# Optimization experiments

Measured on AMD Instinct MI355X. Metric: run time of the kernel, lower is better.

Reference implementation:

```python
import jax, jax.numpy as jnp
import numpy as np

BLANK = 0
B, T, D_TN = 32, 1000, 640
D_PN, D_J, V = 640, 640, 1024


def lstm_step(x, h, c, W_ih, W_hh, b):
    # x:[B,D_PN] h,c:[B,D_PN]
    gates = x @ W_ih.T + h @ W_hh.T + b  # [B,4*D_PN]
    i, f, g, o = jnp.split(gates, 4, axis=-1)
    c_new = jax.nn.sigmoid(f) * c + jax.nn.sigmoid(i) * jnp.tanh(g)
    h_new = jax.nn.sigmoid(o) * jnp.tanh(c_new)
    return h_new, c_new


def setup_inputs() -> dict:
    key = jax.random.key(0)
    ks = jax.random.split(key, 10)
    s_pn = 1.0 / np.sqrt(D_PN)
    s_tn = 1.0 / np.sqrt(D_TN)
    s_j = 1.0 / np.sqrt(D_J)
    return {
        "tn_output": jax.random.normal(ks[0], (B, T, D_TN), jnp.float32),
        "E": jax.random.normal(ks[1], (V, D_PN), jnp.float32) * 0.02,
        "W_ih": jax.random.normal(ks[2], (4 * D_PN, D_PN), jnp.float32) * s_pn,
        "W_hh": jax.random.normal(ks[3], (4 * D_PN, D_PN), jnp.float32) * s_pn,
        "b_lstm": jnp.zeros((4 * D_PN,), jnp.float32),
        "W_tn": jax.random.normal(ks[4], (D_J, D_TN), jnp.float32) * s_tn,
        "W_pn": jax.random.normal(ks[5], (D_J, D_PN), jnp.float32) * s_pn,
        "b_joint": jnp.zeros((D_J,), jnp.float32),
        "W_out": jax.random.normal(ks[6], (V, D_J), jnp.float32) * s_j,
        "b_out": jnp.zeros((V,), jnp.float32),
    }


def reference(tn_output, E, W_ih, W_hh, b_lstm, W_tn, W_pn, b_joint, W_out, b_out):
    """Vectorized transducer greedy decode (beam_size=1 path).
    Returns (emitted_tokens [B,T] (blank where no emission), logp_scores [B],
    mean exp score scalar) mirroring the torch module's greedy output."""
    b, t = tn_output.shape[0], tn_output.shape[1]
    dt = tn_output.dtype
    # initial PN step on initial_token_id (= blank), hidden None -> zeros
    h0 = jnp.zeros((b, W_hh.shape[1]), dt)
    c0 = jnp.zeros((b, W_hh.shape[1]), dt)
    x0 = E[jnp.full((b,), BLANK)]
    h, c = lstm_step(x0, h0, c0, W_ih, W_hh, b_lstm)
    out_pn = h
    # precompute TN projection for the whole utterance: [T,B,D_J]
    tn_proj = jnp.einsum("btd,jd->tbj", tn_output, W_tn)

    def step(state, tn_t):
        h, c, out_pn, last_tok, score = state
        z = jnp.tanh(tn_t + out_pn @ W_pn.T + b_joint)          # [B,D_J]
        logp = jax.nn.log_softmax(z @ W_out.T + b_out, axis=-1)  # [B,V]
        pos = jnp.argmax(logp, axis=-1).astype(jnp.int32)        # [B]
        lp = jnp.take_along_axis(logp, pos[:, None].astype(jnp.int32), axis=-1)[:, 0]
        nonblank = pos != BLANK
        score = score + jnp.where(nonblank, lp, jnp.zeros_like(lp))
        tok = jnp.where(nonblank, pos, last_tok)
        # PN advances only for hyps that emitted a non-blank label
        h2, c2 = lstm_step(E[tok], h, c, W_ih, W_hh, b_lstm)
        m = nonblank[:, None]
        h_n = jnp.where(m, h2, h)
        c_n = jnp.where(m, c2, c)
        out_n = jnp.where(m, h2, out_pn)
        emit = jnp.where(nonblank, pos, jnp.full_like(pos, BLANK))
        return (h_n, c_n, out_n, tok, score), emit

    init = (h, c, out_pn, jnp.full((b,), BLANK, jnp.int32), jnp.zeros((b,), dt))
    (_, _, _, _, score), emits = jax.lax.scan(step, init, tn_proj)
    tokens = jnp.swapaxes(emits, 0, 1)  # [B,T]
    return tokens, score, jnp.exp(score).mean()
```

## Files before the change

### kernel.cpp

```cpp
#include <hip/hip_runtime.h>
#include <stdint.h>


typedef unsigned long long u64;
typedef uint32_t u32;

#define TT 1000
#define DD 640
#define GG 2560
#define VV 1024

#define NA 80
#define NL 64
#define NC 80
#define NBLK (NA + NL + NC)

static constexpr size_t OFF_WTN  = 0;
static constexpr size_t OFF_WPN  = OFF_WTN  + 409600;
static constexpr size_t OFF_WHH  = OFF_WPN  + 409600;
static constexpr size_t OFF_WOUT = OFF_WHH  + 1638400;
static constexpr size_t OFF_P    = OFF_WOUT + 655360;
static constexpr size_t OFF_XH   = OFF_P    + 2621440;
static constexpr size_t OFF_XZ   = OFF_XH   + 40960;
static constexpr size_t OFF_SC   = OFF_XZ   + 20480;
static constexpr size_t OFF_LKEY = OFF_SC   + 32;
static constexpr size_t OFF_LSE  = OFF_LKEY + 4096;
static constexpr size_t OFF_MCFC = OFF_LSE  + 2048;
static constexpr size_t OFF_MCFA = OFF_MCFC + 51200;
static constexpr size_t OFF_MCFL = OFF_MCFA + 20480;
static constexpr size_t OFF_END  = OFF_MCFL + 20480;

__device__ __forceinline__ float sigf(float x) { return 1.0f / (1.0f + expf(-x)); }

__device__ __forceinline__ u32 ordf(float f) {
  u32 u = __float_as_uint(f);
  return (u & 0x80000000u) ? ~u : (u | 0x80000000u);
}

__device__ __forceinline__ void cstore2(float* p, float a, float b) {
  u64 v = ((u64)__float_as_uint(b) << 32) | (u64)__float_as_uint(a);
  __hip_atomic_store((u64*)p, v, __ATOMIC_RELAXED, __HIP_MEMORY_SCOPE_AGENT);
}
__device__ __forceinline__ float2 cload2(const float* p) {
  u64 v = __hip_atomic_load((const u64*)p, __ATOMIC_RELAXED, __HIP_MEMORY_SCOPE_AGENT);
  return make_float2(__uint_as_float((u32)v), __uint_as_float((u32)(v >> 32)));
}
__device__ __forceinline__ u64 cloadu64(const u64* p) {
  return __hip_atomic_load(p, __ATOMIC_RELAXED, __HIP_MEMORY_SCOPE_AGENT);
}
__device__ __forceinline__ void cstoreu64(u64* p, u64 v) {
  __hip_atomic_store(p, v, __ATOMIC_RELAXED, __HIP_MEMORY_SCOPE_AGENT);
}
__device__ __forceinline__ float cloadf(const float* p) {
  return __hip_atomic_load(p, __ATOMIC_RELAXED, __HIP_MEMORY_SCOPE_AGENT);
}
__device__ __forceinline__ void cstoref(float* p, float v) {
  __hip_atomic_store(p, v, __ATOMIC_RELAXED, __HIP_MEMORY_SCOPE_AGENT);
}

__device__ __forceinline__ void wait_mc(const int* mc, int nprod, int target) {
  if ((int)threadIdx.x < nprod) {
    while (__hip_atomic_load(mc + threadIdx.x * 4, __ATOMIC_RELAXED,
                             __HIP_MEMORY_SCOPE_AGENT) < target)
      __builtin_amdgcn_s_sleep(2);
  }
  __syncthreads();
}
__device__ __forceinline__ void publish_mc(int* mc, int ncons, int nprod,
                                           int myprod, int val) {
  __syncthreads();
  if ((int)threadIdx.x < ncons)
    __hip_atomic_store(mc + ((size_t)threadIdx.x * nprod + myprod) * 4, val,
                       __ATOMIC_RELAXED, __HIP_MEMORY_SCOPE_AGENT);
}

__device__ __forceinline__ void fma4(float& a, const float4 w, const float4 x) {
  a = fmaf(w.x, x.x, fmaf(w.y, x.y, fmaf(w.z, x.z, fmaf(w.w, x.w, a))));
}
__device__ __forceinline__ void fma22(float& a, const float4 w, const float2 xa,
                                      const float2 xb) {
  a = fmaf(w.x, xa.x, fmaf(w.y, xa.y, fmaf(w.z, xb.x, fmaf(w.w, xb.y, a))));
}


__global__ __launch_bounds__(256) void k_wt4(const float* __restrict__ W,
                                             float* __restrict__ WT4, int J) {
  __shared__ float tile[64][65];
  int nj = J >> 6;
  int tj = blockIdx.x % nj, tk = blockIdx.x / nj;
  int jb = tj << 6, kb = tk << 6;
  for (int i = threadIdx.x; i < 4096; i += 256) {
    int d = i & 63, j = i >> 6;
    tile[j][d] = W[(size_t)(jb + j) * DD + (kb + d)];
  }
  __syncthreads();
  for (int i = threadIdx.x; i < 1024; i += 256) {
    int j = i & 63, q = i >> 6;
    float4 v = make_float4(tile[j][q * 4], tile[j][q * 4 + 1], tile[j][q * 4 + 2],
                           tile[j][q * 4 + 3]);
    ((float4*)WT4)[(size_t)((kb >> 2) + q) * J + (jb + j)] = v;
  }
}

__global__ __launch_bounds__(256) void k_pgemm(const float* __restrict__ E,
                                               const float* __restrict__ Wih,
                                               float* __restrict__ P) {
  __shared__ float As[16][65], Bs[16][65];
  int vt = blockIdx.x & 15, gt = blockIdx.x >> 4;
  int vb = vt << 6, gb = gt << 6;
  int tv = threadIdx.x & 15, tg = threadIdx.x >> 4;
  float acc[4][4] = {};
  for (int kb = 0; kb < DD; kb += 16) {
    for (int i = threadIdx.x; i < 1024; i += 256) {
      int k = i & 15, x = i >> 4;
      As[k][x] = E[(size_t)(vb + x) * DD + kb + k];
      Bs[k][x] = Wih[(size_t)(gb + x) * DD + kb + k];
    }
    __syncthreads();
#pragma unroll
    for (int k = 0; k < 16; ++k) {
      float av[4], bv[4];
#pragma unroll
      for (int i = 0; i < 4; ++i) av[i] = As[k][tv * 4 + i];
#pragma unroll
      for (int j = 0; j < 4; ++j) bv[j] = Bs[k][tg * 4 + j];
#pragma unroll
      for (int i = 0; i < 4; ++i)
#pragma unroll
        for (int j = 0; j < 4; ++j) acc[i][j] = fmaf(av[i], bv[j], acc[i][j]);
    }
    __syncthreads();
  }
#pragma unroll
  for (int i = 0; i < 4; ++i)
#pragma unroll
    for (int j = 0; j < 4; ++j)
      P[(size_t)(vb + tv * 4 + i) * GG + gb + tg * 4 + j] = acc[i][j];
}

__global__ __launch_bounds__(256) void k_init(float* __restrict__ ws,
                                              const float* __restrict__ bl) {
  const float* P = ws + OFF_P;
  float* XH0 = ws + OFF_XH;
  int tid = blockIdx.x * 256 + threadIdx.x;
  if (tid < DD) {
    int j = tid;
    float gi = P[j] + bl[j];
    float gg = P[1280 + j] + bl[1280 + j];
    float go = P[1920 + j] + bl[1920 + j];
    float c1 = sigf(gi) * tanhf(gg);
    float h1 = sigf(go) * tanhf(c1);
    for (int b = 0; b < 32; ++b) XH0[b * DD + j] = h1;
  }
  int* mc = (int*)(ws + OFF_MCFC);
  for (int i = tid; i < 92160; i += 1024) mc[i] = 0;
}

__global__ __launch_bounds__(256, 1) void k_decode(float* __restrict__ ws,
                                                   const float* __restrict__ tn,
                                                   const float* __restrict__ bl,
                                                   const float* __restrict__ bj,
                                                   const float* __restrict__ bo,
                                                   float* __restrict__ out) {
  const float* WTN = ws + OFF_WTN;
  const float* WPN = ws + OFF_WPN;
  const float* WHH = ws + OFF_WHH;
  const float* WOUT = ws + OFF_WOUT;
  const float* P = ws + OFF_P;
  float* XH = ws + OFF_XH;
  float* XZ = ws + OFF_XZ;
  float* SCg = ws + OFF_SC;
  u64* LKEY = (u64*)(ws + OFF_LKEY);
  float* LSE = ws + OFF_LSE;
  int* MCFC = (int*)(ws + OFF_MCFC);
  int* MCFA = (int*)(ws + OFF_MCFA);
  int* MCFL = (int*)(ws + OFF_MCFL);

  __shared__ float xbuf[32 * 648];
  __shared__ float red[16 * 16 * 33];
  __shared__ float aux[32 * 33];
  __shared__ u64 kred[32 * 9];
  __shared__ float sered[32 * 9];
  __shared__ float c_lds[8 * 33], h_lds[8 * 33];
  __shared__ float sc_lds[32];
  __shared__ int tok_lds[32], nb_lds[32], lt_lds[32];

  const int bid = blockIdx.x, tid = threadIdx.x;
  const int dq = tid >> 4, bp = tid & 15;
  const int d0 = dq * 40, b0 = bp * 2;

  if (bid < NA) {
    const int j0 = bid * 8;
    const int* myFC = MCFC + (size_t)bid * 320;
    for (int t = 0; t < TT; ++t) {
      const int par = t & 1;
      float acc[8][2] = {};
      const float* t0p = tn + ((size_t)b0 * TT + t) * DD + d0;
      const float* t1p = t0p + (size_t)TT * DD;
#pragma unroll 5
      for (int q = 0; q < 10; ++q) {
        float4 x0 = *(const float4*)(t0p + q * 4);
        float4 x1 = *(const float4*)(t1p + q * 4);
        const float4* wt = (const float4*)WTN + (size_t)((d0 + q * 4) >> 2) * DD + j0;
#pragma unroll
        for (int r = 0; r < 8; ++r) {
          fma4(acc[r][0], wt[r], x0);
          fma4(acc[r][1], wt[r], x1);
        }
      }
      wait_mc(myFC, NC, t);
      const float* h0p = XH + (size_t)par * 20480 + (size_t)b0 * DD + d0;
      const float* h1p = h0p + DD;
#pragma unroll 5
      for (int q = 0; q < 10; ++q) {
        float2 a0 = cload2(h0p + q * 4), a1 = cload2(h0p + q * 4 + 2);
        float2 b1 = cload2(h1p + q * 4), b2 = cload2(h1p + q * 4 + 2);
        const float4* wp = (const float4*)WPN + (size_t)((d0 + q * 4) >> 2) * DD + j0;
#pragma unroll
        for (int r = 0; r < 8; ++r) {
          fma22(acc[r][0], wp[r], a0, a1);
          fma22(acc[r][1], wp[r], b1, b2);
        }
      }
#pragma unroll
      for (int r = 0; r < 8; ++r) {
        red[(dq * 8 + r) * 33 + b0] = acc[r][0];
        red[(dq * 8 + r) * 33 + b0 + 1] = acc[r][1];
      }
      __syncthreads();
      {
        int r = tid >> 5, b = tid & 31;
        float s = 0.f;
#pragma unroll
        for (int k = 0; k < 16; ++k) s += red[(k * 8 + r) * 33 + b];
        aux[r * 33 + b] = tanhf(s + bj[j0 + r]);
      }
      __syncthreads();
      if (tid < 128) {
        int jp = tid >> 5, b = tid & 31;
        cstore2(XZ + (size_t)b * DD + j0 + jp * 2, aux[(jp * 2) * 33 + b],
                aux[(jp * 2 + 1) * 33 + b]);
      }
      publish_mc(MCFA, NL, NA, bid, t + 1);
    }
  } else if (bid < NA + NL) {
    const int lb = bid - NA, v0 = lb * 16;
    const int* myFA = MCFA + (size_t)lb * 320;
    for (int t = 0; t < TT; ++t) {
      wait_mc(myFA, NA, t + 1);
      const float* z0p = XZ + (size_t)b0 * DD + d0;
      const float* z1p = z0p + DD;
      float acc[16][2] = {};
#pragma unroll 5
      for (int q = 0; q < 10; ++q) {
        float2 z0a = cload2(z0p + q * 4), z0b = cload2(z0p + q * 4 + 2);
        float2 z1a = cload2(z1p + q * 4), z1b = cload2(z1p + q * 4 + 2);
        const float4* wo = (const float4*)WOUT + (size_t)((d0 + q * 4) >> 2) * VV + v0;
#pragma unroll
        for (int r = 0; r < 16; ++r) {
          float4 w = wo[r];
          fma22(acc[r][0], w, z0a, z0b);
          fma22(acc[r][1], w, z1a, z1b);
        }
      }
#pragma unroll
      for (int r = 0; r < 16; ++r) {
        red[(dq * 16 + r) * 33 + b0] = acc[r][0];
        red[(dq * 16 + r) * 33 + b0 + 1] = acc[r][1];
      }
      __syncthreads();
#pragma unroll
      for (int o = tid; o < 512; o += 256) {
        int r = o >> 5, b = o & 31;
        float s = bo[v0 + r];
#pragma unroll
        for (int k = 0; k < 16; ++k) s += red[(k * 16 + r) * 33 + b];
        aux[r * 33 + b] = s;
      }
      __syncthreads();
      if (tid < 32) {
        int b = tid;
        float m = -1e30f, se = 0.f;
        int vbest = 0;
#pragma unroll
        for (int r = 0; r < 16; ++r) {
          float x = aux[r * 33 + b];
          se += expf(x);
          if (x > m) { m = x; vbest = r; }
        }
        u64 key = ((u64)ordf(m) << 32) | (u64)(0xFFFFFFFFu - (u32)(v0 + vbest));
        cstoreu64(&LKEY[(size_t)b * 64 + lb], key);
        cstoref(&LSE[(size_t)b * 64 + lb], se);
      }
      publish_mc(MCFL, NC, NL, lb, t + 1);
    }
  } else {
    const int cb = bid - (NA + NL), j0 = cb * 8;
    const int* myFC = MCFC + (size_t)(NA + cb) * 320;
    const int* myFL = MCFL + (size_t)cb * 256;
    {
      int jj = tid >> 5, b = tid & 31, j = j0 + jj;
      float gi = P[j] + bl[j];
      float gg = P[1280 + j] + bl[1280 + j];
      float go = P[1920 + j] + bl[1920 + j];
      float c1 = sigf(gi) * tanhf(gg);
      c_lds[jj * 33 + b] = c1;
      h_lds[jj * 33 + b] = sigf(go) * tanhf(c1);
    }
    if (tid < 32) { lt_lds[tid] = 0; sc_lds[tid] = 0.f; }
    __syncthreads();
    for (int t = 0; t < TT; ++t) {
      const int par = t & 1;
      wait_mc(myFC, NC, t);
      {
        const float* h0p = XH + (size_t)par * 20480 + (size_t)b0 * DD + d0;
        const float* h1p = h0p + DD;
#pragma unroll 5
        for (int q = 0; q < 10; ++q) {
          float2 a0 = cload2(h0p + q * 4), a1 = cload2(h0p + q * 4 + 2);
          float2 b1 = cload2(h1p + q * 4), b2 = cload2(h1p + q * 4 + 2);
          *(float4*)&xbuf[b0 * 648 + d0 + q * 4] = make_float4(a0.x, a0.y, a1.x, a1.y);
          *(float4*)&xbuf[(b0 + 1) * 648 + d0 + q * 4] = make_float4(b1.x, b1.y, b2.x, b2.y);
        }
      }
      __syncthreads();
#pragma unroll
      for (int p = 0; p < 2; ++p) {
        float acc[16][2] = {};
#pragma unroll 5
        for (int q = 0; q < 10; ++q) {
          const int d = d0 + q * 4;
          float4 h0 = *(const float4*)&xbuf[b0 * 648 + d];
          float4 h1 = *(const float4*)&xbuf[(b0 + 1) * 648 + d];
          const float4* wa =
              (const float4*)WHH + (size_t)(d >> 2) * GG + (2 * p) * DD + j0;
          const float4* wb = wa + DD;
#pragma unroll
          for (int jj = 0; jj < 8; ++jj) {
            fma4(acc[jj][0], wa[jj], h0);
            fma4(acc[jj][1], wa[jj], h1);
            fma4(acc[8 + jj][0], wb[jj], h0);
            fma4(acc[8 + jj][1], wb[jj], h1);
          }
        }
#pragma unroll
        for (int r = 0; r < 16; ++r) {
          red[(dq * 16 + r) * 33 + b0] = acc[r][0];
          red[(dq * 16 + r) * 33 + b0 + 1] = acc[r][1];
        }
        __syncthreads();
#pragma unroll
        for (int o = tid; o < 512; o += 256) {
          int r16 = o >> 5, b = o & 31;
          float s = 0.f;
#pragma unroll
          for (int k = 0; k < 16; ++k) s += red[(k * 16 + r16) * 33 + b];
          int g = 2 * p + (r16 >> 3), jj = r16 & 7;
          aux[(g * 8 + jj) * 33 + b] = s;
        }
        __syncthreads();
      }
      wait_mc(myFL, NL, t + 1);
      {
        int b = tid >> 3, ch = tid & 7;
        const u64* kp = LKEY + (size_t)b * 64 + ch * 8;
        u64 km = 0;
#pragma unroll
        for (int i = 0; i < 8; ++i) {
          u64 x = cloadu64(kp + i);
          km = x > km ? x : km;
        }
        kred[b * 9 + ch] = km;
        if (cb == 0) {
          const float* sp = LSE + (size_t)b * 64 + ch * 8;
          float ss = 0.f;
#pragma unroll
          for (int i = 0; i < 8; ++i) ss += cloadf(sp + i);
          sered[b * 9 + ch] = ss;
        }
      }
      __syncthreads();
      if (tid < 32) {
        int b = tid;
        u64 km = 0;
#pragma unroll
        for (int ch = 0; ch < 8; ++ch) {
          u64 x = kred[b * 9 + ch];
          km = x > km ? x : km;
        }
        u32 ou = (u32)(km >> 32);
        u32 fb = (ou & 0x80000000u) ? (ou & 0x7FFFFFFFu) : ~ou;
        float m = __uint_as_float(fb);
        int v = (int)(0xFFFFFFFFu - (u32)(km & 0xFFFFFFFFull));
        int nb = (v != 0) ? 1 : 0;
        int tok = nb ? v : lt_lds[b];
        lt_lds[b] = tok;
        tok_lds[b] = tok;
        nb_lds[b] = nb;
        if (cb == 0) {
          float S = 0.f;
#pragma unroll
          for (int ch = 0; ch < 8; ++ch) S += sered[b * 9 + ch];
          float lp = m - logf(S);
          if (nb) sc_lds[b] += lp;
          out[(size_t)b * TT + t] = nb ? (float)v : 0.0f;
          if (t == TT - 1) SCg[b] = sc_lds[b];
        }
      }
      __syncthreads();
      {
        int jj = tid >> 5, b = tid & 31, j = j0 + jj;
        if (nb_lds[b]) {
          const float* Pr = P + (size_t)tok_lds[b] * GG;
          float gi = aux[(0 + jj) * 33 + b] + Pr[j] + bl[j];
          float gf = aux[(8 + jj) * 33 + b] + Pr[640 + j] + bl[640 + j];
          float gg = aux[(16 + jj) * 33 + b] + Pr[1280 + j] + bl[1280 + j];
          float go = aux[(24 + jj) * 33 + b] + Pr[1920 + j] + bl[1920 + j];
          float c = c_lds[jj * 33 + b];
          float cn = sigf(gf) * c + sigf(gi) * tanhf(gg);
          float hn = sigf(go) * tanhf(cn);
          c_lds[jj * 33 + b] = cn;
          h_lds[jj * 33 + b] = hn;
        }
      }
      __syncthreads();
      if (tid < 128) {
        int jp = tid >> 5, b = tid & 31;
        cstore2(XH + (size_t)(1 - par) * 20480 + (size_t)b * DD + j0 + jp * 2,
                h_lds[(jp * 2) * 33 + b], h_lds[(jp * 2 + 1) * 33 + b]);
      }
      publish_mc(MCFC, NA + NC, NC, cb, t + 1);
    }
  }
}

__global__ __launch_bounds__(64) void k_final(const float* __restrict__ ws,
                                              float* __restrict__ out) {
  __shared__ float sh[32];
  int t = threadIdx.x;
  if (t < 32) {
    float s = ws[OFF_SC + t];
    out[32000 + t] = s;
    sh[t] = expf(s);
  }
  __syncthreads();
  if (t == 0) {
    float a = 0.f;
    for (int i = 0; i < 32; ++i) a += sh[i];
    out[32032] = a / 32.0f;
  }
}

extern "C" void kernel_launch(void* const* d_in, const int* in_sizes, int n_in,
                              void* d_out, int out_size, void* d_ws, size_t ws_size,
                              hipStream_t stream) {
  const float* tn = (const float*)d_in[0];
  const float* E = (const float*)d_in[1];
  const float* Wih = (const float*)d_in[2];
  const float* Whh = (const float*)d_in[3];
  const float* bl = (const float*)d_in[4];
  const float* Wtn = (const float*)d_in[5];
  const float* Wpn = (const float*)d_in[6];
  const float* bj = (const float*)d_in[7];
  const float* Wout = (const float*)d_in[8];
  const float* bo = (const float*)d_in[9];
  float* ws = (float*)d_ws;
  float* out = (float*)d_out;

  k_wt4<<<100, 256, 0, stream>>>(Wtn, ws + OFF_WTN, DD);
  k_wt4<<<100, 256, 0, stream>>>(Wpn, ws + OFF_WPN, DD);
  k_wt4<<<400, 256, 0, stream>>>(Whh, ws + OFF_WHH, GG);
  k_wt4<<<160, 256, 0, stream>>>(Wout, ws + OFF_WOUT, VV);
  k_pgemm<<<640, 256, 0, stream>>>(E, Wih, ws + OFF_P);
  k_init<<<4, 256, 0, stream>>>(ws, bl);
  k_decode<<<NBLK, 256, 0, stream>>>(ws, tn, bl, bj, bo, out);
  k_final<<<1, 64, 0, stream>>>(ws, out);
}
```

Baseline: 26.95 ms.

## Merge joint-projection blocks into LSTM blocks and split across more blocks

Removes the separate joint (A) block group and folds the tn/pn joint projection into the LSTM (C) blocks, now 160 blocks each owning 4 hidden units instead of 8. The tn projection for the next step is computed off the critical path while waiting for logits, and the W_hh gate computation follows the z publish so it overlaps with the logit blocks. LDS reduction indices are skewed to avoid bank conflicts. This trades one inter-block handoff per step for more blocks in the flag-based barrier, and larger flag arrays.

New measurement: 31.02 ms. 15.1% more time.

```diff
diff --git a/kernel.cpp b/kernel.cpp
--- a/kernel.cpp
+++ b/kernel.cpp
@@ -10,10 +10,9 @@
 #define GG 2560
 #define VV 1024
 
-#define NA 80
+#define NC 160
 #define NL 64
-#define NC 80
-#define NBLK (NA + NL + NC)
+#define NBLK (NC + NL)
 
 static constexpr size_t OFF_WTN  = 0;
 static constexpr size_t OFF_WPN  = OFF_WTN  + 409600;
@@ -26,9 +25,9 @@
 static constexpr size_t OFF_LKEY = OFF_SC   + 32;
 static constexpr size_t OFF_LSE  = OFF_LKEY + 4096;
 static constexpr size_t OFF_MCFC = OFF_LSE  + 2048;
-static constexpr size_t OFF_MCFA = OFF_MCFC + 51200;
-static constexpr size_t OFF_MCFL = OFF_MCFA + 20480;
-static constexpr size_t OFF_END  = OFF_MCFL + 20480;
+static constexpr size_t OFF_MCFZ = OFF_MCFC + 102400;
+static constexpr size_t OFF_MCFL = OFF_MCFZ + 40960;
+static constexpr size_t OFF_END  = OFF_MCFL + 40960;
 
 __device__ __forceinline__ float sigf(float x) { return 1.0f / (1.0f + expf(-x)); }
 
@@ -153,7 +152,7 @@
     for (int b = 0; b < 32; ++b) XH0[b * DD + j] = h1;
   }
   int* mc = (int*)(ws + OFF_MCFC);
-  for (int i = tid; i < 92160; i += 1024) mc[i] = 0;
+  for (int i = tid; i < 184320; i += 1024) mc[i] = 0;
 }
 
 __global__ __launch_bounds__(256, 1) void k_decode(float* __restrict__ ws,
@@ -173,7 +172,7 @@
   u64* LKEY = (u64*)(ws + OFF_LKEY);
   float* LSE = ws + OFF_LSE;
   int* MCFC = (int*)(ws + OFF_MCFC);
-  int* MCFA = (int*)(ws + OFF_MCFA);
+  int* MCFZ = (int*)(ws + OFF_MCFZ);
   int* MCFL = (int*)(ws + OFF_MCFL);
 
   __shared__ float xbuf[32 * 648];
@@ -181,7 +180,7 @@
   __shared__ float aux[32 * 33];
   __shared__ u64 kred[32 * 9];
   __shared__ float sered[32 * 9];
-  __shared__ float c_lds[8 * 33], h_lds[8 * 33];
+  __shared__ float c_lds[4 * 33], h_lds[4 * 33];
   __shared__ float sc_lds[32];
   __shared__ int tok_lds[32], nb_lds[32], lt_lds[32];
 
@@ -189,13 +188,27 @@
   const int dq = tid >> 4, bp = tid & 15;
   const int d0 = dq * 40, b0 = bp * 2;
 
-  if (bid < NA) {
-    const int j0 = bid * 8;
-    const int* myFC = MCFC + (size_t)bid * 320;
-    for (int t = 0; t < TT; ++t) {
-      const int par = t & 1;
-      float acc[8][2] = {};
-      const float* t0p = tn + ((size_t)b0 * TT + t) * DD + d0;
+  if (bid < NC) {
+    const int cb = bid, j0 = cb * 4;
+    const int* myFC = MCFC + (size_t)cb * 640;
+    const int* myFL = MCFL + (size_t)cb * 256;
+    {
+      int jj = (tid >> 5) & 3, b = tid & 31, j = j0 + jj;
+      if (tid < 128) {
+        float gi = P[j] + bl[j];
+        float gg = P[1280 + j] + bl[1280 + j];
+        float go = P[1920 + j] + bl[1920 + j];
+        float c1 = sigf(gi) * tanhf(gg);
+        c_lds[jj * 33 + b] = c1;
+        h_lds[jj * 33 + b] = sigf(go) * tanhf(c1);
+      }
+    }
+    if (tid < 32) { lt_lds[tid] = 0; sc_lds[tid] = 0.f; }
+    float acc_tn[4][2];
+#pragma unroll
+    for (int r = 0; r < 4; ++r) acc_tn[r][0] = acc_tn[r][1] = 0.f;
+    {
+      const float* t0p = tn + ((size_t)b0 * TT + 0) * DD + d0;
       const float* t1p = t0p + (size_t)TT * DD;
 #pragma unroll 5
       for (int q = 0; q < 10; ++q) {
@@ -203,116 +216,23 @@
         float4 x1 = *(const float4*)(t1p + q * 4);
         const float4* wt = (const float4*)WTN + (size_t)((d0 + q * 4) >> 2) * DD + j0;
 #pragma unroll
-        for (int r = 0; r < 8; ++r) {
-          fma4(acc[r][0], wt[r], x0);
-          fma4(acc[r][1], wt[r], x1);
-        }
-      }
-      wait_mc(myFC, NC, t);
-      const float* h0p = XH + (size_t)par * 20480 + (size_t)b0 * DD + d0;
-      const float* h1p = h0p + DD;
-#pragma unroll 5
-      for (int q = 0; q < 10; ++q) {
-        float2 a0 = cload2(h0p + q * 4), a1 = cload2(h0p + q * 4 + 2);
-        float2 b1 = cload2(h1p + q * 4), b2 = cload2(h1p + q * 4 + 2);
-        const float4* wp = (const float4*)WPN + (size_t)((d0 + q * 4) >> 2) * DD + j0;
-#pragma unroll
-        for (int r = 0; r < 8; ++r) {
-          fma22(acc[r][0], wp[r], a0, a1);
-          fma22(acc[r][1], wp[r], b1, b2);
-        }
-      }
-#pragma unroll
-      for (int r = 0; r < 8; ++r) {
-        red[(dq * 8 + r) * 33 + b0] = acc[r][0];
-        red[(dq * 8 + r) * 33 + b0 + 1] = acc[r][1];
-      }
-      __syncthreads();
-      {
-        int r = tid >> 5, b = tid & 31;
-        float s = 0.f;
-#pragma unroll
-        for (int k = 0; k < 16; ++k) s += red[(k * 8 + r) * 33 + b];
-        aux[r * 33 + b] = tanhf(s + bj[j0 + r]);
-      }
-      __syncthreads();
-      if (tid < 128) {
-        int jp = tid >> 5, b = tid & 31;
-        cstore2(XZ + (size_t)b * DD + j0 + jp * 2, aux[(jp * 2) * 33 + b],
-                aux[(jp * 2 + 1) * 33 + b]);
-      }
-      publish_mc(MCFA, NL, NA, bid, t + 1);
-    }
-  } else if (bid < NA + NL) {
-    const int lb = bid - NA, v0 = lb * 16;
-    const int* myFA = MCFA + (size_t)lb * 320;
-    for (int t = 0; t < TT; ++t) {
-      wait_mc(myFA, NA, t + 1);
-      const float* z0p = XZ + (size_t)b0 * DD + d0;
-      const float* z1p = z0p + DD;
-      float acc[16][2] = {};
-#pragma unroll 5
-      for (int q = 0; q < 10; ++q) {
-        float2 z0a = cload2(z0p + q * 4), z0b = cload2(z0p + q * 4 + 2);
-        float2 z1a = cload2(z1p + q * 4), z1b = cload2(z1p + q * 4 + 2);
-        const float4* wo = (const float4*)WOUT + (size_t)((d0 + q * 4) >> 2) * VV + v0;
-#pragma unroll
-        for (int r = 0; r < 16; ++r) {
-          float4 w = wo[r];
-          fma22(acc[r][0], w, z0a, z0b);
-          fma22(acc[r][1], w, z1a, z1b);
-        }
-      }
-#pragma unroll
-      for (int r = 0; r < 16; ++r) {
-        red[(dq * 16 + r) * 33 + b0] = acc[r][0];
-        red[(dq * 16 + r) * 33 + b0 + 1] = acc[r][1];
-      }
-      __syncthreads();
-#pragma unroll
-      for (int o = tid; o < 512; o += 256) {
-        int r = o >> 5, b = o & 31;
-        float s = bo[v0 + r];
-#pragma unroll
-        for (int k = 0; k < 16; ++k) s += red[(k * 16 + r) * 33 + b];
-        aux[r * 33 + b] = s;
-      }
-      __syncthreads();
-      if (tid < 32) {
-        int b = tid;
-        float m = -1e30f, se = 0.f;
-        int vbest = 0;
-#pragma unroll
-        for (int r = 0; r < 16; ++r) {
-          float x = aux[r * 33 + b];
-          se += expf(x);
-          if (x > m) { m = x; vbest = r; }
-        }
-        u64 key = ((u64)ordf(m) << 32) | (u64)(0xFFFFFFFFu - (u32)(v0 + vbest));
-        cstoreu64(&LKEY[(size_t)b * 64 + lb], key);
-        cstoref(&LSE[(size_t)b * 64 + lb], se);
-      }
-      publish_mc(MCFL, NC, NL, lb, t + 1);
-    }
-  } else {
-    const int cb = bid - (NA + NL), j0 = cb * 8;
-    const int* myFC = MCFC + (size_t)(NA + cb) * 320;
-    const int* myFL = MCFL + (size_t)cb * 256;
-    {
-      int jj = tid >> 5, b = tid & 31, j = j0 + jj;
-      float gi = P[j] + bl[j];
-      float gg = P[1280 + j] + bl[1280 + j];
-      float go = P[1920 + j] + bl[1920 + j];
-      float c1 = sigf(gi) * tanhf(gg);
-      c_lds[jj * 33 + b] = c1;
-      h_lds[jj * 33 + b] = sigf(go) * tanhf(c1);
-    }
-    if (tid < 32) { lt_lds[tid] = 0; sc_lds[tid] = 0.f; }
+        for (int r = 0; r < 4; ++r) {
+          fma4(acc_tn[r][0], wt[r], x0);
+          fma4(acc_tn[r][1], wt[r], x1);
+        }
+      }
+    }
     __syncthreads();
     for (int t = 0; t < TT; ++t) {
       const int par = t & 1;
       wait_mc(myFC, NC, t);
       {
+        float acc[4][2];
+#pragma unroll
+        for (int r = 0; r < 4; ++r) {
+          acc[r][0] = acc_tn[r][0];
+          acc[r][1] = acc_tn[r][1];
+        }
         const float* h0p = XH + (size_t)par * 20480 + (size_t)b0 * DD + d0;
         const float* h1p = h0p + DD;
 #pragma unroll 5
@@ -321,44 +241,83 @@
           float2 b1 = cload2(h1p + q * 4), b2 = cload2(h1p + q * 4 + 2);
           *(float4*)&xbuf[b0 * 648 + d0 + q * 4] = make_float4(a0.x, a0.y, a1.x, a1.y);
           *(float4*)&xbuf[(b0 + 1) * 648 + d0 + q * 4] = make_float4(b1.x, b1.y, b2.x, b2.y);
-        }
-      }
-      __syncthreads();
-#pragma unroll
-      for (int p = 0; p < 2; ++p) {
+          const float4* wp = (const float4*)WPN + (size_t)((d0 + q * 4) >> 2) * DD + j0;
+#pragma unroll
+          for (int r = 0; r < 4; ++r) {
+            fma22(acc[r][0], wp[r], a0, a1);
+            fma22(acc[r][1], wp[r], b1, b2);
+          }
+        }
+#pragma unroll
+        for (int r = 0; r < 4; ++r) {
+          red[(dq * 4 + r) * 33 + ((b0 + dq) & 31)] = acc[r][0];
+          red[(dq * 4 + r) * 33 + ((b0 + 1 + dq) & 31)] = acc[r][1];
+        }
+      }
+      __syncthreads();
+      if (tid < 128) {
+        int r = tid >> 5, b = tid & 31;
+        float s = 0.f;
+#pragma unroll
+        for (int k = 0; k < 16; ++k) s += red[(k * 4 + r) * 33 + ((b + k) & 31)];
+        aux[r * 33 + b] = tanhf(s + bj[j0 + r]);
+      }
+      __syncthreads();
+      if (tid < 64) {
+        int jp = tid >> 5, b = tid & 31;
+        cstore2(XZ + (size_t)b * DD + j0 + jp * 2, aux[(jp * 2) * 33 + b],
+                aux[(jp * 2 + 1) * 33 + b]);
+      }
+      publish_mc(MCFZ, NL, NC, cb, t + 1);
+      {
         float acc[16][2] = {};
 #pragma unroll 5
         for (int q = 0; q < 10; ++q) {
           const int d = d0 + q * 4;
           float4 h0 = *(const float4*)&xbuf[b0 * 648 + d];
           float4 h1 = *(const float4*)&xbuf[(b0 + 1) * 648 + d];
-          const float4* wa =
-              (const float4*)WHH + (size_t)(d >> 2) * GG + (2 * p) * DD + j0;
-          const float4* wb = wa + DD;
-#pragma unroll
-          for (int jj = 0; jj < 8; ++jj) {
-            fma4(acc[jj][0], wa[jj], h0);
-            fma4(acc[jj][1], wa[jj], h1);
-            fma4(acc[8 + jj][0], wb[jj], h0);
-            fma4(acc[8 + jj][1], wb[jj], h1);
+          const float4* w0 = (const float4*)WHH + (size_t)(d >> 2) * GG + j0;
+#pragma unroll
+          for (int g = 0; g < 4; ++g) {
+            const float4* wg = w0 + g * DD;
+#pragma unroll
+            for (int jj = 0; jj < 4; ++jj) {
+              fma4(acc[g * 4 + jj][0], wg[jj], h0);
+              fma4(acc[g * 4 + jj][1], wg[jj], h1);
+            }
           }
         }
 #pragma unroll
         for (int r = 0; r < 16; ++r) {
-          red[(dq * 16 + r) * 33 + b0] = acc[r][0];
-          red[(dq * 16 + r) * 33 + b0 + 1] = acc[r][1];
-        }
-        __syncthreads();
-#pragma unroll
-        for (int o = tid; o < 512; o += 256) {
-          int r16 = o >> 5, b = o & 31;
-          float s = 0.f;
-#pragma unroll
-          for (int k = 0; k < 16; ++k) s += red[(k * 16 + r16) * 33 + b];
-          int g = 2 * p + (r16 >> 3), jj = r16 & 7;
-          aux[(g * 8 + jj) * 33 + b] = s;
-        }
-        __syncthreads();
+          red[(dq * 16 + r) * 33 + ((b0 + dq) & 31)] = acc[r][0];
+          red[(dq * 16 + r) * 33 + ((b0 + 1 + dq) & 31)] = acc[r][1];
+        }
+      }
+      __syncthreads();
+#pragma unroll
+      for (int o = tid; o < 512; o += 256) {
+        int r16 = o >> 5, b = o & 31;
+        float s = 0.f;
+#pragma unroll
+        for (int k = 0; k < 16; ++k) s += red[(k * 16 + r16) * 33 + ((b + k) & 31)];
+        aux[r16 * 33 + b] = s;
+      }
+      if (t + 1 < TT) {
+#pragma unroll
+        for (int r = 0; r < 4; ++r) acc_tn[r][0] = acc_tn[r][1] = 0.f;
+        const float* t0p = tn + ((size_t)b0 * TT + (t + 1)) * DD + d0;
+        const float* t1p = t0p + (size_t)TT * DD;
+#pragma unroll 5
+        for (int q = 0; q < 10; ++q) {
+          float4 x0 = *(const float4*)(t0p + q * 4);
+          float4 x1 = *(const float4*)(t1p + q * 4);
+          const float4* wt = (const float4*)WTN + (size_t)((d0 + q * 4) >> 2) * DD + j0;
+#pragma unroll
+          for (int r = 0; r < 4; ++r) {
+            fma4(acc_tn[r][0], wt[r], x0);
+            fma4(acc_tn[r][1], wt[r], x1);
+          }
+        }
       }
       wait_mc(myFL, NL, t + 1);
       {
@@ -408,14 +367,14 @@
         }
       }
       __syncthreads();
-      {
+      if (tid < 128) {
         int jj = tid >> 5, b = tid & 31, j = j0 + jj;
         if (nb_lds[b]) {
           const float* Pr = P + (size_t)tok_lds[b] * GG;
           float gi = aux[(0 + jj) * 33 + b] + Pr[j] + bl[j];
-          float gf = aux[(8 + jj) * 33 + b] + Pr[640 + j] + bl[640 + j];
-          float gg = aux[(16 + jj) * 33 + b] + Pr[1280 + j] + bl[1280 + j];
-          float go = aux[(24 + jj) * 33 + b] + Pr[1920 + j] + bl[1920 + j];
+          float gf = aux[(4 + jj) * 33 + b] + Pr[640 + j] + bl[640 + j];
+          float gg = aux[(8 + jj) * 33 + b] + Pr[1280 + j] + bl[1280 + j];
+          float go = aux[(12 + jj) * 33 + b] + Pr[1920 + j] + bl[1920 + j];
           float c = c_lds[jj * 33 + b];
           float cn = sigf(gf) * c + sigf(gi) * tanhf(gg);
           float hn = sigf(go) * tanhf(cn);
@@ -424,12 +383,63 @@
         }
       }
       __syncthreads();
-      if (tid < 128) {
+      if (tid < 64) {
         int jp = tid >> 5, b = tid & 31;
         cstore2(XH + (size_t)(1 - par) * 20480 + (size_t)b * DD + j0 + jp * 2,
                 h_lds[(jp * 2) * 33 + b], h_lds[(jp * 2 + 1) * 33 + b]);
       }
-      publish_mc(MCFC, NA + NC, NC, cb, t + 1);
+      publish_mc(MCFC, NC, NC, cb, t + 1);
+    }
+  } else {
+    const int lb = bid - NC, v0 = lb * 16;
+    const int* myFZ = MCFZ + (size_t)lb * 640;
+    for (int t = 0; t < TT; ++t) {
+      wait_mc(myFZ, NC, t + 1);
+      const float* z0p = XZ + (size_t)b0 * DD + d0;
+      const float* z1p = z0p + DD;
+      float acc[16][2] = {};
+#pragma unroll 5
+      for (int q = 0; q < 10; ++q) {
+        float2 z0a = cload2(z0p + q * 4), z0b = cload2(z0p + q * 4 + 2);
+        float2 z1a = cload2(z1p + q * 4), z1b = cload2(z1p + q * 4 + 2);
+        const float4* wo = (const float4*)WOUT + (size_t)((d0 + q * 4) >> 2) * VV + v0;
+#pragma unroll
+        for (int r = 0; r < 16; ++r) {
+          float4 w = wo[r];
+          fma22(acc[r][0], w, z0a, z0b);
+          fma22(acc[r][1], w, z1a, z1b);
+        }
+      }
+#pragma unroll
+      for (int r = 0; r < 16; ++r) {
+        red[(dq * 16 + r) * 33 + ((b0 + dq) & 31)] = acc[r][0];
+        red[(dq * 16 + r) * 33 + ((b0 + 1 + dq) & 31)] = acc[r][1];
+      }
+      __syncthreads();
+#pragma unroll
+      for (int o = tid; o < 512; o += 256) {
+        int r = o >> 5, b = o & 31;
+        float s = bo[v0 + r];
+#pragma unroll
+        for (int k = 0; k < 16; ++k) s += red[(k * 16 + r) * 33 + ((b + k) & 31)];
+        aux[r * 33 + b] = s;
+      }
+      __syncthreads();
+      if (tid < 32) {
+        int b = tid;
+        float m = -1e30f, se = 0.f;
+        int vbest = 0;
+#pragma unroll
+        for (int r = 0; r < 16; ++r) {
+          float x = aux[r * 33 + b];
+          se += expf(x);
+          if (x > m) { m = x; vbest = r; }
+        }
+        u64 key = ((u64)ordf(m) << 32) | (u64)(0xFFFFFFFFu - (u32)(v0 + vbest));
+        cstoreu64(&LKEY[(size_t)b * 64 + lb], key);
+        cstoref(&LSE[(size_t)b * 64 + lb], se);
+      }
+      publish_mc(MCFL, NC, NL, lb, t + 1);
     }
   }
 }
```

## Replace per-producer flag barriers with epoch-tagged data words for inter-block sync

Applied to the files above, without the earlier changes.

Removes the separate flag arrays and wait/publish handshakes between the joint, output and LSTM block groups. Each published value is now a 64-bit word carrying its float and the timestep epoch, and consumers speculatively compute on loaded data, retrying with a short sleep until every epoch tag matches. This drops a flag round-trip and barrier per stage per timestep, at the cost of doubling the bytes moved for the hidden and joint vectors, recomputing partial dot products on retry, and relying on the argmax key packing a 10-bit timestep. The joint buffer is double-buffered so producers cannot overwrite data still being read.

New measurement: 86.31 ms. 220% more time.

```diff
diff --git a/kernel.cpp b/kernel.cpp
--- a/kernel.cpp
+++ b/kernel.cpp
@@ -21,14 +21,11 @@
 static constexpr size_t OFF_WOUT = OFF_WHH  + 1638400;
 static constexpr size_t OFF_P    = OFF_WOUT + 655360;
 static constexpr size_t OFF_XH   = OFF_P    + 2621440;
-static constexpr size_t OFF_XZ   = OFF_XH   + 40960;
-static constexpr size_t OFF_SC   = OFF_XZ   + 20480;
+static constexpr size_t OFF_XZ   = OFF_XH   + 81920;
+static constexpr size_t OFF_SC   = OFF_XZ   + 81920;
 static constexpr size_t OFF_LKEY = OFF_SC   + 32;
 static constexpr size_t OFF_LSE  = OFF_LKEY + 4096;
-static constexpr size_t OFF_MCFC = OFF_LSE  + 2048;
-static constexpr size_t OFF_MCFA = OFF_MCFC + 51200;
-static constexpr size_t OFF_MCFL = OFF_MCFA + 20480;
-static constexpr size_t OFF_END  = OFF_MCFL + 20480;
+static constexpr size_t OFF_END  = OFF_LSE  + 4096;
 
 __device__ __forceinline__ float sigf(float x) { return 1.0f / (1.0f + expf(-x)); }
 
@@ -37,42 +34,17 @@
   return (u & 0x80000000u) ? ~u : (u | 0x80000000u);
 }
 
-__device__ __forceinline__ void cstore2(float* p, float a, float b) {
-  u64 v = ((u64)__float_as_uint(b) << 32) | (u64)__float_as_uint(a);
-  __hip_atomic_store((u64*)p, v, __ATOMIC_RELAXED, __HIP_MEMORY_SCOPE_AGENT);
-}
-__device__ __forceinline__ float2 cload2(const float* p) {
-  u64 v = __hip_atomic_load((const u64*)p, __ATOMIC_RELAXED, __HIP_MEMORY_SCOPE_AGENT);
-  return make_float2(__uint_as_float((u32)v), __uint_as_float((u32)(v >> 32)));
-}
 __device__ __forceinline__ u64 cloadu64(const u64* p) {
   return __hip_atomic_load(p, __ATOMIC_RELAXED, __HIP_MEMORY_SCOPE_AGENT);
 }
 __device__ __forceinline__ void cstoreu64(u64* p, u64 v) {
   __hip_atomic_store(p, v, __ATOMIC_RELAXED, __HIP_MEMORY_SCOPE_AGENT);
 }
-__device__ __forceinline__ float cloadf(const float* p) {
-  return __hip_atomic_load(p, __ATOMIC_RELAXED, __HIP_MEMORY_SCOPE_AGENT);
-}
-__device__ __forceinline__ void cstoref(float* p, float v) {
-  __hip_atomic_store(p, v, __ATOMIC_RELAXED, __HIP_MEMORY_SCOPE_AGENT);
-}
-
-__device__ __forceinline__ void wait_mc(const int* mc, int nprod, int target) {
-  if ((int)threadIdx.x < nprod) {
-    while (__hip_atomic_load(mc + threadIdx.x * 4, __ATOMIC_RELAXED,
-                             __HIP_MEMORY_SCOPE_AGENT) < target)
-      __builtin_amdgcn_s_sleep(2);
-  }
-  __syncthreads();
-}
-__device__ __forceinline__ void publish_mc(int* mc, int ncons, int nprod,
-                                           int myprod, int val) {
-  __syncthreads();
-  if ((int)threadIdx.x < ncons)
-    __hip_atomic_store(mc + ((size_t)threadIdx.x * nprod + myprod) * 4, val,
-                       __ATOMIC_RELAXED, __HIP_MEMORY_SCOPE_AGENT);
-}
+__device__ __forceinline__ u64 packfe(float f, int e) {
+  return ((u64)(u32)e << 32) | (u64)__float_as_uint(f);
+}
+__device__ __forceinline__ float valof(u64 w) { return __uint_as_float((u32)w); }
+__device__ __forceinline__ int epof(u64 w) { return (int)(u32)(w >> 32); }
 
 __device__ __forceinline__ void fma4(float& a, const float4 w, const float4 x) {
   a = fmaf(w.x, x.x, fmaf(w.y, x.y, fmaf(w.z, x.z, fmaf(w.w, x.w, a))));
@@ -141,7 +113,10 @@
 __global__ __launch_bounds__(256) void k_init(float* __restrict__ ws,
                                               const float* __restrict__ bl) {
   const float* P = ws + OFF_P;
-  float* XH0 = ws + OFF_XH;
+  u64* XHu = (u64*)(ws + OFF_XH);
+  u64* XZu = (u64*)(ws + OFF_XZ);
+  u64* LKu = (u64*)(ws + OFF_LKEY);
+  u64* LSu = (u64*)(ws + OFF_LSE);
   int tid = blockIdx.x * 256 + threadIdx.x;
   if (tid < DD) {
     int j = tid;
@@ -150,10 +125,13 @@
     float go = P[1920 + j] + bl[1920 + j];
     float c1 = sigf(gi) * tanhf(gg);
     float h1 = sigf(go) * tanhf(c1);
-    for (int b = 0; b < 32; ++b) XH0[b * DD + j] = h1;
-  }
-  int* mc = (int*)(ws + OFF_MCFC);
-  for (int i = tid; i < 92160; i += 1024) mc[i] = 0;
+    for (int b = 0; b < 32; ++b) XHu[(size_t)b * 640 + j] = packfe(h1, 0);
+  }
+  const u64 inval = packfe(0.f, -1);
+  for (int i = tid; i < 20480; i += 1024) XHu[20480 + i] = inval;
+  for (int i = tid; i < 40960; i += 1024) XZu[i] = inval;
+  for (int i = tid; i < 2048; i += 1024) LKu[i] = 0x3FFull;
+  for (int i = tid; i < 2048; i += 1024) LSu[i] = inval;
 }
 
 __global__ __launch_bounds__(256, 1) void k_decode(float* __restrict__ ws,
@@ -167,14 +145,11 @@
   const float* WHH = ws + OFF_WHH;
   const float* WOUT = ws + OFF_WOUT;
   const float* P = ws + OFF_P;
-  float* XH = ws + OFF_XH;
-  float* XZ = ws + OFF_XZ;
+  u64* XHu = (u64*)(ws + OFF_XH);
+  u64* XZu = (u64*)(ws + OFF_XZ);
   float* SCg = ws + OFF_SC;
-  u64* LKEY = (u64*)(ws + OFF_LKEY);
-  float* LSE = ws + OFF_LSE;
-  int* MCFC = (int*)(ws + OFF_MCFC);
-  int* MCFA = (int*)(ws + OFF_MCFA);
-  int* MCFL = (int*)(ws + OFF_MCFL);
+  u64* LKu = (u64*)(ws + OFF_LKEY);
+  u64* LSu = (u64*)(ws + OFF_LSE);
 
   __shared__ float xbuf[32 * 648];
   __shared__ float red[16 * 16 * 33];
@@ -191,10 +166,9 @@
 
   if (bid < NA) {
     const int j0 = bid * 8;
-    const int* myFC = MCFC + (size_t)bid * 320;
     for (int t = 0; t < TT; ++t) {
       const int par = t & 1;
-      float acc[8][2] = {};
+      float acc_tn[8][2] = {};
       const float* t0p = tn + ((size_t)b0 * TT + t) * DD + d0;
       const float* t1p = t0p + (size_t)TT * DD;
 #pragma unroll 5
@@ -204,23 +178,44 @@
         const float4* wt = (const float4*)WTN + (size_t)((d0 + q * 4) >> 2) * DD + j0;
 #pragma unroll
         for (int r = 0; r < 8; ++r) {
-          fma4(acc[r][0], wt[r], x0);
-          fma4(acc[r][1], wt[r], x1);
-        }
-      }
-      wait_mc(myFC, NC, t);
-      const float* h0p = XH + (size_t)par * 20480 + (size_t)b0 * DD + d0;
-      const float* h1p = h0p + DD;
+          fma4(acc_tn[r][0], wt[r], x0);
+          fma4(acc_tn[r][1], wt[r], x1);
+        }
+      }
+      const u64* h0p = XHu + (size_t)par * 20480 + (size_t)b0 * 640 + d0;
+      const u64* h1p = h0p + 640;
+      float acc[8][2];
+      for (;;) {
+        u32 bad = 0;
+#pragma unroll
+        for (int r = 0; r < 8; ++r) {
+          acc[r][0] = acc_tn[r][0];
+          acc[r][1] = acc_tn[r][1];
+        }
 #pragma unroll 5
-      for (int q = 0; q < 10; ++q) {
-        float2 a0 = cload2(h0p + q * 4), a1 = cload2(h0p + q * 4 + 2);
-        float2 b1 = cload2(h1p + q * 4), b2 = cload2(h1p + q * 4 + 2);
-        const float4* wp = (const float4*)WPN + (size_t)((d0 + q * 4) >> 2) * DD + j0;
-#pragma unroll
-        for (int r = 0; r < 8; ++r) {
-          fma22(acc[r][0], wp[r], a0, a1);
-          fma22(acc[r][1], wp[r], b1, b2);
-        }
+        for (int q = 0; q < 10; ++q) {
+          u64 w0 = cloadu64(h0p + q * 4), w1 = cloadu64(h0p + q * 4 + 1);
+          u64 w2 = cloadu64(h0p + q * 4 + 2), w3 = cloadu64(h0p + q * 4 + 3);
+          u64 y0 = cloadu64(h1p + q * 4), y1 = cloadu64(h1p + q * 4 + 1);
+          u64 y2 = cloadu64(h1p + q * 4 + 2), y3 = cloadu64(h1p + q * 4 + 3);
+          bad |= (u32)(epof(w0) != t) | (u32)(epof(w1) != t) |
+                 (u32)(epof(w2) != t) | (u32)(epof(w3) != t) |
+                 (u32)(epof(y0) != t) | (u32)(epof(y1) != t) |
+                 (u32)(epof(y2) != t) | (u32)(epof(y3) != t);
+          float2 a0 = make_float2(valof(w0), valof(w1));
+          float2 a1 = make_float2(valof(w2), valof(w3));
+          float2 b1 = make_float2(valof(y0), valof(y1));
+          float2 b2 = make_float2(valof(y2), valof(y3));
+          const float4* wp =
+              (const float4*)WPN + (size_t)((d0 + q * 4) >> 2) * DD + j0;
+#pragma unroll
+          for (int r = 0; r < 8; ++r) {
+            fma22(acc[r][0], wp[r], a0, a1);
+            fma22(acc[r][1], wp[r], b1, b2);
+          }
+        }
+        if (!bad) break;
+        __builtin_amdgcn_s_sleep(2);
       }
 #pragma unroll
       for (int r = 0; r < 8; ++r) {
@@ -238,30 +233,47 @@
       __syncthreads();
       if (tid < 128) {
         int jp = tid >> 5, b = tid & 31;
-        cstore2(XZ + (size_t)b * DD + j0 + jp * 2, aux[(jp * 2) * 33 + b],
-                aux[(jp * 2 + 1) * 33 + b]);
-      }
-      publish_mc(MCFA, NL, NA, bid, t + 1);
+        u64* zp = XZu + (size_t)par * 20480 + (size_t)b * 640 + j0 + jp * 2;
+        cstoreu64(zp, packfe(aux[(jp * 2) * 33 + b], t));
+        cstoreu64(zp + 1, packfe(aux[(jp * 2 + 1) * 33 + b], t));
+      }
     }
   } else if (bid < NA + NL) {
     const int lb = bid - NA, v0 = lb * 16;
-    const int* myFA = MCFA + (size_t)lb * 320;
     for (int t = 0; t < TT; ++t) {
-      wait_mc(myFA, NA, t + 1);
-      const float* z0p = XZ + (size_t)b0 * DD + d0;
-      const float* z1p = z0p + DD;
-      float acc[16][2] = {};
+      const int par = t & 1;
+      const u64* z0p = XZu + (size_t)par * 20480 + (size_t)b0 * 640 + d0;
+      const u64* z1p = z0p + 640;
+      float acc[16][2];
+      for (;;) {
+        u32 bad = 0;
+#pragma unroll
+        for (int r = 0; r < 16; ++r) acc[r][0] = acc[r][1] = 0.f;
 #pragma unroll 5
-      for (int q = 0; q < 10; ++q) {
-        float2 z0a = cload2(z0p + q * 4), z0b = cload2(z0p + q * 4 + 2);
-        float2 z1a = cload2(z1p + q * 4), z1b = cload2(z1p + q * 4 + 2);
-        const float4* wo = (const float4*)WOUT + (size_t)((d0 + q * 4) >> 2) * VV + v0;
-#pragma unroll
-        for (int r = 0; r < 16; ++r) {
-          float4 w = wo[r];
-          fma22(acc[r][0], w, z0a, z0b);
-          fma22(acc[r][1], w, z1a, z1b);
-        }
+        for (int q = 0; q < 10; ++q) {
+          u64 w0 = cloadu64(z0p + q * 4), w1 = cloadu64(z0p + q * 4 + 1);
+          u64 w2 = cloadu64(z0p + q * 4 + 2), w3 = cloadu64(z0p + q * 4 + 3);
+          u64 y0 = cloadu64(z1p + q * 4), y1 = cloadu64(z1p + q * 4 + 1);
+          u64 y2 = cloadu64(z1p + q * 4 + 2), y3 = cloadu64(z1p + q * 4 + 3);
+          bad |= (u32)(epof(w0) != t) | (u32)(epof(w1) != t) |
+                 (u32)(epof(w2) != t) | (u32)(epof(w3) != t) |
+                 (u32)(epof(y0) != t) | (u32)(epof(y1) != t) |
+                 (u32)(epof(y2) != t) | (u32)(epof(y3) != t);
+          float2 z0a = make_float2(valof(w0), valof(w1));
+          float2 z0b = make_float2(valof(w2), valof(w3));
+          float2 z1a = make_float2(valof(y0), valof(y1));
+          float2 z1b = make_float2(valof(y2), valof(y3));
+          const float4* wo =
+              (const float4*)WOUT + (size_t)((d0 + q * 4) >> 2) * VV + v0;
+#pragma unroll
+          for (int r = 0; r < 16; ++r) {
+            float4 w = wo[r];
+            fma22(acc[r][0], w, z0a, z0b);
+            fma22(acc[r][1], w, z1a, z1b);
+          }
+        }
+        if (!bad) break;
+        __builtin_amdgcn_s_sleep(2);
       }
 #pragma unroll
       for (int r = 0; r < 16; ++r) {
@@ -288,16 +300,14 @@
           se += expf(x);
           if (x > m) { m = x; vbest = r; }
         }
-        u64 key = ((u64)ordf(m) << 32) | (u64)(0xFFFFFFFFu - (u32)(v0 + vbest));
-        cstoreu64(&LKEY[(size_t)b * 64 + lb], key);
-        cstoref(&LSE[(size_t)b * 64 + lb], se);
-      }
-      publish_mc(MCFL, NC, NL, lb, t + 1);
+        u64 key = ((u64)ordf(m) << 32) | ((u64)(1023 - (v0 + vbest)) << 20) |
+                  (u64)t;
+        cstoreu64(&LKu[(size_t)b * 64 + lb], key);
+        cstoreu64(&LSu[(size_t)b * 64 + lb], packfe(se, t));
+      }
     }
   } else {
     const int cb = bid - (NA + NL), j0 = cb * 8;
-    const int* myFC = MCFC + (size_t)(NA + cb) * 320;
-    const int* myFL = MCFL + (size_t)cb * 256;
     {
       int jj = tid >> 5, b = tid & 31, j = j0 + jj;
       float gi = P[j] + bl[j];
@@ -311,17 +321,27 @@
     __syncthreads();
     for (int t = 0; t < TT; ++t) {
       const int par = t & 1;
-      wait_mc(myFC, NC, t);
-      {
-        const float* h0p = XH + (size_t)par * 20480 + (size_t)b0 * DD + d0;
-        const float* h1p = h0p + DD;
+      const u64* h0p = XHu + (size_t)par * 20480 + (size_t)b0 * 640 + d0;
+      const u64* h1p = h0p + 640;
+      for (;;) {
+        u32 bad = 0;
 #pragma unroll 5
         for (int q = 0; q < 10; ++q) {
-          float2 a0 = cload2(h0p + q * 4), a1 = cload2(h0p + q * 4 + 2);
-          float2 b1 = cload2(h1p + q * 4), b2 = cload2(h1p + q * 4 + 2);
-          *(float4*)&xbuf[b0 * 648 + d0 + q * 4] = make_float4(a0.x, a0.y, a1.x, a1.y);
-          *(float4*)&xbuf[(b0 + 1) * 648 + d0 + q * 4] = make_float4(b1.x, b1.y, b2.x, b2.y);
-        }
+          u64 w0 = cloadu64(h0p + q * 4), w1 = cloadu64(h0p + q * 4 + 1);
+          u64 w2 = cloadu64(h0p + q * 4 + 2), w3 = cloadu64(h0p + q * 4 + 3);
+          u64 y0 = cloadu64(h1p + q * 4), y1 = cloadu64(h1p + q * 4 + 1);
+          u64 y2 = cloadu64(h1p + q * 4 + 2), y3 = cloadu64(h1p + q * 4 + 3);
+          bad |= (u32)(epof(w0) != t) | (u32)(epof(w1) != t) |
+                 (u32)(epof(w2) != t) | (u32)(epof(w3) != t) |
+                 (u32)(epof(y0) != t) | (u32)(epof(y1) != t) |
+                 (u32)(epof(y2) != t) | (u32)(epof(y3) != t);
+          *(float4*)&xbuf[b0 * 648 + d0 + q * 4] =
+              make_float4(valof(w0), valof(w1), valof(w2), valof(w3));
+          *(float4*)&xbuf[(b0 + 1) * 648 + d0 + q * 4] =
+              make_float4(valof(y0), valof(y1), valof(y2), valof(y3));
+        }
+        if (!bad) break;
+        __builtin_amdgcn_s_sleep(2);
       }
       __syncthreads();
 #pragma unroll
@@ -360,24 +380,35 @@
         }
         __syncthreads();
       }
-      wait_mc(myFL, NL, t + 1);
       {
         int b = tid >> 3, ch = tid & 7;
-        const u64* kp = LKEY + (size_t)b * 64 + ch * 8;
-        u64 km = 0;
-#pragma unroll
-        for (int i = 0; i < 8; ++i) {
-          u64 x = cloadu64(kp + i);
-          km = x > km ? x : km;
+        const u64* kp = LKu + (size_t)b * 64 + ch * 8;
+        const u64* sp = LSu + (size_t)b * 64 + ch * 8;
+        u64 km;
+        float ss;
+        for (;;) {
+          u32 bad = 0;
+          km = 0;
+          ss = 0.f;
+#pragma unroll
+          for (int i = 0; i < 8; ++i) {
+            u64 x = cloadu64(kp + i);
+            bad |= (u32)((x & 0x3FFull) != (u64)t);
+            km = x > km ? x : km;
+          }
+          if (cb == 0) {
+#pragma unroll
+            for (int i = 0; i < 8; ++i) {
+              u64 w = cloadu64(sp + i);
+              bad |= (u32)(epof(w) != t);
+              ss += valof(w);
+            }
+          }
+          if (!bad) break;
+          __builtin_amdgcn_s_sleep(2);
         }
         kred[b * 9 + ch] = km;
-        if (cb == 0) {
-          const float* sp = LSE + (size_t)b * 64 + ch * 8;
-          float ss = 0.f;
-#pragma unroll
-          for (int i = 0; i < 8; ++i) ss += cloadf(sp + i);
-          sered[b * 9 + ch] = ss;
-        }
+        if (cb == 0) sered[b * 9 + ch] = ss;
       }
       __syncthreads();
       if (tid < 32) {
@@ -391,7 +422,7 @@
         u32 ou = (u32)(km >> 32);
         u32 fb = (ou & 0x80000000u) ? (ou & 0x7FFFFFFFu) : ~ou;
         float m = __uint_as_float(fb);
-        int v = (int)(0xFFFFFFFFu - (u32)(km & 0xFFFFFFFFull));
+        int v = 1023 - (int)((km >> 20) & 0x3FF);
         int nb = (v != 0) ? 1 : 0;
         int tok = nb ? v : lt_lds[b];
         lt_lds[b] = tok;
@@ -426,10 +457,10 @@
       __syncthreads();
       if (tid < 128) {
         int jp = tid >> 5, b = tid & 31;
-        cstore2(XH + (size_t)(1 - par) * 20480 + (size_t)b * DD + j0 + jp * 2,
-                h_lds[(jp * 2) * 33 + b], h_lds[(jp * 2 + 1) * 33 + b]);
-      }
-      publish_mc(MCFC, NA + NC, NC, cb, t + 1);
+        u64* hp = XHu + (size_t)(1 - par) * 20480 + (size_t)b * 640 + j0 + jp * 2;
+        cstoreu64(hp, packfe(h_lds[(jp * 2) * 33 + b], t + 1));
+        cstoreu64(hp + 1, packfe(h_lds[(jp * 2 + 1) * 33 + b], t + 1));
+      }
     }
   }
 }
```
